# Optimization experiments

Hardware: AMD Instinct MI355X
Metric: run time of the kernel (lower is better)

## Reference

```python
import jax, jax.numpy as jnp
import numpy as np

D_MODEL = 1024
N_HEADS = 16
HEAD_DIM = D_MODEL // N_HEADS
BATCH = 2
SEQ = 2048


def setup_inputs() -> dict:
    key = jax.random.key(0)
    ks = jax.random.split(key, 9)
    s = 1.0 / np.sqrt(D_MODEL)
    x = jax.random.normal(ks[0], (BATCH, SEQ, D_MODEL), dtype=jnp.float32)
    # causal mask, broadcastable to (B, H, S, S); positions with 0 are masked out
    mask = jnp.tril(jnp.ones((SEQ, SEQ), dtype=bool))[None, None, :, :]
    Wq = jax.random.normal(ks[1], (D_MODEL, D_MODEL), dtype=jnp.float32) * s
    Wk = jax.random.normal(ks[2], (D_MODEL, D_MODEL), dtype=jnp.float32) * s
    Wv = jax.random.normal(ks[3], (D_MODEL, D_MODEL), dtype=jnp.float32) * s
    Wo = jax.random.normal(ks[4], (D_MODEL, D_MODEL), dtype=jnp.float32) * s
    bq = jnp.zeros((D_MODEL,), jnp.float32)
    bk = jnp.zeros((D_MODEL,), jnp.float32)
    bv = jnp.zeros((D_MODEL,), jnp.float32)
    bo = jnp.zeros((D_MODEL,), jnp.float32)
    return {"x": x, "mask": mask, "Wq": Wq, "bq": bq, "Wk": Wk, "bk": bk,
            "Wv": Wv, "bv": bv, "Wo": Wo, "bo": bo}


def reference(x, mask, Wq, bq, Wk, bk, Wv, bv, Wo, bo):
    B, S, _ = x.shape
    scale = HEAD_DIM ** -0.5
    # nn.Linear: y = x @ W.T + b ; W stored as (out, in)
    def proj(W, b):
        y = jnp.einsum('bsd,ed->bse', x, W) + b
        return y.reshape(B, S, N_HEADS, HEAD_DIM).transpose(0, 2, 1, 3)  # (B,H,S,Dh)
    q = proj(Wq, bq)
    k = proj(Wk, bk)
    v = proj(Wv, bv)
    scores = jnp.einsum('bhqd,bhkd->bhqk', q, k) * scale  # (B,H,S,S)
    scores = jnp.where(mask, scores, jnp.float32(-jnp.inf))
    weights = jax.nn.softmax(scores, axis=-1)
    attn = jnp.einsum('bhqk,bhkd->bhqd', weights, v)
    attn = attn.transpose(0, 2, 1, 3).reshape(B, S, D_MODEL)
    out = jnp.einsum('bsd,ed->bse', attn, Wo) + bo
    return out
```

## Files before the change

kernel.cpp:

```cpp
#include <hip/hip_runtime.h>
#include <hip/hip_bf16.h>

using bf16x8 = __attribute__((ext_vector_type(8))) short;
using f32x4  = __attribute__((ext_vector_type(4))) float;

#define SEQ      2048
#define DMODEL   1024
#define NHEADS   16
#define HDIM     64
#define MROWS    4096

__device__ __forceinline__ unsigned short f2bf(float f) {
  union { float f; unsigned u; } c; c.f = f;
  unsigned r = c.u + 0x7FFFu + ((c.u >> 16) & 1u);
  return (unsigned short)(r >> 16);
}

__device__ __forceinline__ unsigned cvtpk(float a, float b) {
  unsigned r;
  asm("v_cvt_pk_bf16_f32 %0, %1, %2" : "=v"(r) : "v"(a), "v"(b));
  return r;
}

__device__ __forceinline__ float fexp2(float x) {
  float r;
  asm("v_exp_f32 %0, %1" : "=v"(r) : "v"(x));
  return r;
}

__device__ __forceinline__ void gload16(const void* g, void* s) {
  __builtin_amdgcn_global_load_lds(
      (const __attribute__((address_space(1))) void*)g,
      (__attribute__((address_space(3))) void*)s, 16, 0, 0);
}

__global__ void cvt_all(const float* __restrict__ x,  const float* __restrict__ wq,
                        const float* __restrict__ wk, const float* __restrict__ wv,
                        const float* __restrict__ wo,
                        unsigned short* __restrict__ xb,  unsigned short* __restrict__ wqb,
                        unsigned short* __restrict__ wkb, unsigned short* __restrict__ wvb,
                        unsigned short* __restrict__ wob)
{
  int i = blockIdx.x * blockDim.x + threadIdx.x;
  const float* src; unsigned short* dst; int off;
  if (i < 1048576) { src = x; dst = xb; off = i; }
  else {
    int k = i - 1048576, seg = k >> 18; off = k & 262143;
    if      (seg == 0) { src = wq; dst = wqb; }
    else if (seg == 1) { src = wk; dst = wkb; }
    else if (seg == 2) { src = wv; dst = wvb; }
    else               { src = wo; dst = wob; }
  }
  const float4 v = ((const float4*)src)[off];
  ushort4 o;
  o.x = f2bf(v.x); o.y = f2bf(v.y); o.z = f2bf(v.z); o.w = f2bf(v.w);
  ((ushort4*)dst)[off] = o;
}

__global__ __launch_bounds__(256, 4)
void gemm_qkv(const unsigned short* __restrict__ Ab,
              const unsigned short* __restrict__ Wqb,
              const unsigned short* __restrict__ Wkb,
              const unsigned short* __restrict__ Wvb,
              const float* __restrict__ bq, const float* __restrict__ bk,
              const float* __restrict__ bv,
              unsigned short* __restrict__ Qo, unsigned short* __restrict__ Ko,
              unsigned short* __restrict__ Vto)
{
  __shared__ unsigned short Sbuf[2][128 * 64];
  unsigned short* As = Sbuf[0];
  unsigned short* Bs = Sbuf[1];
  const int t  = threadIdx.x;
  const int w  = t >> 6, l = t & 63;
  const int lr = l & 15, lg = l >> 4;
  const int bm = blockIdx.x / 24;
  const int bn = blockIdx.x % 24;
  const int which = bn >> 3;
  const unsigned short* Bsrc = which == 0 ? Wqb : (which == 1 ? Wkb : Wvb);
  const float* biasp = which == 0 ? bq : (which == 1 ? bk : bv);
  const int bnw = bn & 7;
  const int wm = w >> 1, wn = w & 1;

  const char* Agp = (const char*)Ab + (size_t)bm * 128 * 2048;
  const char* Bgp = (const char*)Bsrc + (size_t)bnw * 128 * 2048;

  f32x4 acc[4][4];
  #pragma unroll
  for (int a = 0; a < 4; ++a)
    #pragma unroll
    for (int b = 0; b < 4; ++b) acc[a][b] = (f32x4){0.f, 0.f, 0.f, 0.f};

  for (int kt = 0; kt < 16; ++kt) {
    const int kbyte = kt * 128;
    #pragma unroll
    for (int i = 0; i < 4; ++i) {
      int idx  = i * 256 + t;
      int row  = idx >> 3;
      int colb = (idx & 7) << 4;
      int scol = colb ^ ((row & 7) << 4);
      gload16(Agp + (size_t)row * 2048 + kbyte + scol, (char*)As + idx * 16);
      gload16(Bgp + (size_t)row * 2048 + kbyte + scol, (char*)Bs + idx * 16);
    }
    __syncthreads();
    #pragma unroll
    for (int kk = 0; kk < 2; ++kk) {
      bf16x8 af[4], bfr[4];
      #pragma unroll
      for (int x = 0; x < 4; ++x) {
        int ra = wm * 64 + x * 16 + lr;
        int rb = wn * 64 + x * 16 + lr;
        int cb = (kk * 64 + lg * 16) ^ ((lr & 7) << 4);
        af[x]  = *(const bf16x8*)((const char*)As + ra * 128 + cb);
        bfr[x] = *(const bf16x8*)((const char*)Bs + rb * 128 + cb);
      }
      #pragma unroll
      for (int xa = 0; xa < 4; ++xa)
        #pragma unroll
        for (int xb = 0; xb < 4; ++xb)
          acc[xa][xb] = __builtin_amdgcn_mfma_f32_16x16x32_bf16(af[xa], bfr[xb], acc[xa][xb], 0, 0, 0);
    }
    __syncthreads();
  }

  if (which == 2) {
    char* T = (char*)Sbuf;
    #pragma unroll
    for (int xb = 0; xb < 4; ++xb) {
      int col = wn * 64 + xb * 16 + lr;
      float biasv = biasp[bnw * 128 + col];
      #pragma unroll
      for (int xa = 0; xa < 4; ++xa) {
        int row0 = wm * 64 + xa * 16 + lg * 4;
        uint2 pk;
        pk.x = cvtpk(acc[xa][xb][0] + biasv, acc[xa][xb][1] + biasv);
        pk.y = cvtpk(acc[xa][xb][2] + biasv, acc[xa][xb][3] + biasv);
        *(uint2*)(T + col * 256 + (((row0 >> 3) ^ (col & 7)) << 4) + ((row0 & 7) << 1)) = pk;
      }
    }
    __syncthreads();
    const int bb = bm >> 4;
    const int s_base = (bm & 15) * 128;
    #pragma unroll
    for (int it = 0; it < 8; ++it) {
      int idx = it * 256 + t;
      int c   = idx >> 4;
      int sc  = idx & 15;
      uint4 v = *(const uint4*)(T + c * 256 + ((sc ^ (c & 7)) << 4));
      int colg = bnw * 128 + c;
      int h = colg >> 6, dh = colg & 63;
      int s0 = s_base + sc * 8;
      *(uint4*)&Vto[(((size_t)(bb * NHEADS + h)) * HDIM + dh) * SEQ + s0] = v;
    }
  } else {
    #pragma unroll
    for (int xb = 0; xb < 4; ++xb) {
      int colg = bnw * 128 + wn * 64 + xb * 16 + lr;
      int h  = colg >> 6, dh = colg & 63;
      float biasv = biasp[colg];
      #pragma unroll
      for (int xa = 0; xa < 4; ++xa) {
        int row0 = bm * 128 + wm * 64 + xa * 16 + lg * 4;
        #pragma unroll
        for (int i = 0; i < 4; ++i) {
          int m = row0 + i;
          int b = m >> 11, s = m & 2047;
          float v = acc[xa][xb][i] + biasv;
          if (which == 0)
            Qo[(((size_t)(b * NHEADS + h)) * SEQ + s) * HDIM + dh] = f2bf(v * 0.180336881f);
          else
            Ko[(((size_t)(b * NHEADS + h)) * SEQ + s) * HDIM + dh] = f2bf(v);
        }
      }
    }
  }
}

__device__ __forceinline__ void stage_kv64(const char* Kg, const char* Vg,
                                           char* Kl, char* Vl, int nb, int t)
{
  #pragma unroll
  for (int i = 0; i < 2; ++i) {
    int idx = i * 256 + t;
    int row = idx >> 3, colb = (idx & 7) << 4;
    int scol = colb ^ ((row & 7) << 4);
    gload16(Kg + (size_t)(nb + row) * 128 + scol, Kl + idx * 16);
    gload16(Vg + (size_t)row * 4096 + (size_t)nb * 2 + scol, Vl + idx * 16);
  }
}

__device__ __forceinline__ void attn_sub16(const char* Kl, const char* Vl, char* Pw,
                                           const bf16x8 (&qf)[2], const bf16x8 ones,
                                           f32x4 (&o)[4], f32x4 &accL,
                                           int q0w, int kbase, bool diag, int lr, int lg)
{
  bf16x8 kf[4][2];
  #pragma unroll
  for (int n = 0; n < 4; ++n)
    #pragma unroll
    for (int kk = 0; kk < 2; ++kk)
      kf[n][kk] = *(const bf16x8*)(Kl + (size_t)(n * 16 + lr) * 128 +
                                   ((kk * 64 + lg * 16) ^ ((lr & 7) << 4)));
  f32x4 st[4];
  __builtin_amdgcn_s_setprio(1);
  #pragma unroll
  for (int n = 0; n < 4; ++n) {
    f32x4 acc = (f32x4){0.f, 0.f, 0.f, 0.f};
    #pragma unroll
    for (int kk = 0; kk < 2; ++kk)
      acc = __builtin_amdgcn_mfma_f32_16x16x32_bf16(kf[n][kk], qf[kk], acc, 0, 0, 0);
    st[n] = acc;
  }
  __builtin_amdgcn_s_setprio(0);
  if (diag) {
    #pragma unroll
    for (int n = 0; n < 4; ++n) {
      #pragma unroll
      for (int i = 0; i < 4; ++i) {
        int key = kbase + n * 16 + lg * 4 + i;
        if (key > q0w + lr) st[n][i] = -3.0e38f;
      }
    }
  }
  #pragma unroll
  for (int n = 0; n < 4; ++n) {
    float p0 = fexp2(st[n][0]);
    float p1 = fexp2(st[n][1]);
    float p2 = fexp2(st[n][2]);
    float p3 = fexp2(st[n][3]);
    uint2 pw;
    pw.x = cvtpk(p0, p1);
    pw.y = cvtpk(p2, p3);
    *(uint2*)(Pw + lr * 128 + ((n * 32 + lg * 8) ^ ((lr & 7) << 4))) = pw;
  }
  __builtin_amdgcn_s_setprio(1);
  #pragma unroll
  for (int kk = 0; kk < 2; ++kk) {
    bf16x8 af = *(const bf16x8*)(Pw + lr * 128 + ((kk * 64 + lg * 16) ^ ((lr & 7) << 4)));
    accL = __builtin_amdgcn_mfma_f32_16x16x32_bf16(af, ones, accL, 0, 0, 0);
    #pragma unroll
    for (int n = 0; n < 4; ++n) {
      bf16x8 vf = *(const bf16x8*)(Vl + (size_t)(n * 16 + lr) * 128 +
                    ((kk * 64 + lg * 16) ^ ((lr & 7) << 4)));
      o[n] = __builtin_amdgcn_mfma_f32_16x16x32_bf16(af, vf, o[n], 0, 0, 0);
    }
  }
  __builtin_amdgcn_s_setprio(0);
}

__global__ __launch_bounds__(256, 2)
void attn_fwd(const unsigned short* __restrict__ Q,
              const unsigned short* __restrict__ K,
              const unsigned short* __restrict__ Vt,
              unsigned short* __restrict__ O)
{
  const int t = threadIdx.x;
  const int w = t >> 6, l = t & 63;
  const int lr = l & 15, lg = l >> 4;
  const int bh = blockIdx.x & 31;
  const int p  = blockIdx.x >> 5;
  const int qtA = p, qtB = 31 - p;
  const int b = bh >> 4, h = bh & 15;
  const int q0wA = qtA * 64 + w * 16;
  const int q0wB = qtB * 64 + w * 16;

  const unsigned short* Qp = Q + (size_t)bh * SEQ * HDIM;
  const char* Kg = (const char*)(K  + (size_t)bh * SEQ * HDIM);
  const char* Vg = (const char*)(Vt + (size_t)bh * HDIM * SEQ);

  __shared__ unsigned short Klds[2][64 * 64];
  __shared__ unsigned short Vlds[2][64 * 64];
  __shared__ unsigned short Plds[4][16][64];
  char* Pw = (char*)Plds[w];

  bf16x8 qfA[2], qfB[2];
  #pragma unroll
  for (int kk = 0; kk < 2; ++kk) {
    qfA[kk] = *(const bf16x8*)(Qp + (size_t)(q0wA + lr) * HDIM + kk * 32 + lg * 8);
    qfB[kk] = *(const bf16x8*)(Qp + (size_t)(q0wB + lr) * HDIM + kk * 32 + lg * 8);
  }

  bf16x8 ones;
  #pragma unroll
  for (int e = 0; e < 8; ++e) ones[e] = (short)0x3F80;

  f32x4 oA[4], oB[4];
  f32x4 accLA = (f32x4){0.f, 0.f, 0.f, 0.f};
  f32x4 accLB = (f32x4){0.f, 0.f, 0.f, 0.f};
  #pragma unroll
  for (int n = 0; n < 4; ++n) {
    oA[n] = (f32x4){0.f, 0.f, 0.f, 0.f};
    oB[n] = (f32x4){0.f, 0.f, 0.f, 0.f};
  }

  stage_kv64(Kg, Vg, (char*)Klds[0], (char*)Vlds[0], 0, t);
  {
    int kb1 = (1 <= qtA) ? 1 : 0;
    stage_kv64(Kg, Vg, (char*)Klds[1], (char*)Vlds[1], kb1 * 64, t);
  }

  int cur = 0;
  for (int j = 0; j < 33; ++j) {
    if (j < 32)
      asm volatile("s_waitcnt vmcnt(4)" ::: "memory");
    else
      asm volatile("s_waitcnt vmcnt(0)" ::: "memory");
    __builtin_amdgcn_s_barrier();
    asm volatile("" ::: "memory");
    if (j <= qtA) {
      attn_sub16((const char*)Klds[cur], (const char*)Vlds[cur], Pw, qfA, ones,
                 oA, accLA, q0wA, j * 64, j == qtA, lr, lg);
    } else {
      int kb = j - qtA - 1;
      attn_sub16((const char*)Klds[cur], (const char*)Vlds[cur], Pw, qfB, ones,
                 oB, accLB, q0wB, kb * 64, j == 32, lr, lg);
    }
    asm volatile("" ::: "memory");
    __builtin_amdgcn_s_barrier();
    asm volatile("" ::: "memory");
    if (j + 2 < 33) {
      int jn = j + 2;
      int kbn = (jn <= qtA) ? jn : jn - qtA - 1;
      stage_kv64(Kg, Vg, (char*)Klds[cur], (char*)Vlds[cur], kbn * 64, t);
    }
    cur ^= 1;
  }

  #pragma unroll
  for (int n = 0; n < 4; ++n) {
    int col = h * HDIM + n * 16 + lr;
    #pragma unroll
    for (int i = 0; i < 4; ++i) {
      int srowA = q0wA + lg * 4 + i;
      int srowB = q0wB + lg * 4 + i;
      O[((size_t)(b * SEQ + srowA)) * DMODEL + col] = f2bf(oA[n][i] / accLA[i]);
      O[((size_t)(b * SEQ + srowB)) * DMODEL + col] = f2bf(oB[n][i] / accLB[i]);
    }
  }
}

__global__ __launch_bounds__(256, 2)
void gemm_out(const unsigned short* __restrict__ Ab, const unsigned short* __restrict__ Bb,
              const float* __restrict__ bias, float* __restrict__ C)
{
  __shared__ unsigned short As[128 * 64];
  __shared__ unsigned short Bs[64 * 64];
  const int t  = threadIdx.x;
  const int w  = t >> 6, l = t & 63;
  const int lr = l & 15, lg = l >> 4;
  const int bm = blockIdx.x >> 4;
  const int bn = blockIdx.x & 15;
  const int wm = w >> 1, wn = w & 1;

  const char* Agp = (const char*)Ab + (size_t)bm * 128 * 2048;
  const char* Bgp = (const char*)Bb + (size_t)bn * 64 * 2048;

  f32x4 acc[4][2];
  #pragma unroll
  for (int a = 0; a < 4; ++a)
    #pragma unroll
    for (int b = 0; b < 2; ++b) acc[a][b] = (f32x4){0.f, 0.f, 0.f, 0.f};

  for (int kt = 0; kt < 16; ++kt) {
    const int kbyte = kt * 128;
    #pragma unroll
    for (int i = 0; i < 4; ++i) {
      int idx  = i * 256 + t;
      int row  = idx >> 3;
      int colb = (idx & 7) << 4;
      int scol = colb ^ ((row & 7) << 4);
      gload16(Agp + (size_t)row * 2048 + kbyte + scol, (char*)As + idx * 16);
    }
    #pragma unroll
    for (int i = 0; i < 2; ++i) {
      int idx  = i * 256 + t;
      int row  = idx >> 3;
      int colb = (idx & 7) << 4;
      int scol = colb ^ ((row & 7) << 4);
      gload16(Bgp + (size_t)row * 2048 + kbyte + scol, (char*)Bs + idx * 16);
    }
    __syncthreads();
    #pragma unroll
    for (int kk = 0; kk < 2; ++kk) {
      bf16x8 af[4], bfr[2];
      #pragma unroll
      for (int x = 0; x < 4; ++x) {
        int ra = wm * 64 + x * 16 + lr;
        int cb = (kk * 64 + lg * 16) ^ ((lr & 7) << 4);
        af[x]  = *(const bf16x8*)((const char*)As + ra * 128 + cb);
      }
      #pragma unroll
      for (int x = 0; x < 2; ++x) {
        int rb = wn * 32 + x * 16 + lr;
        int cb = (kk * 64 + lg * 16) ^ ((lr & 7) << 4);
        bfr[x] = *(const bf16x8*)((const char*)Bs + rb * 128 + cb);
      }
      #pragma unroll
      for (int xa = 0; xa < 4; ++xa)
        #pragma unroll
        for (int xb = 0; xb < 2; ++xb)
          acc[xa][xb] = __builtin_amdgcn_mfma_f32_16x16x32_bf16(af[xa], bfr[xb], acc[xa][xb], 0, 0, 0);
    }
    __syncthreads();
  }
  #pragma unroll
  for (int xb = 0; xb < 2; ++xb) {
    int col = bn * 64 + wn * 32 + xb * 16 + lr;
    float bvv = bias[col];
    #pragma unroll
    for (int xa = 0; xa < 4; ++xa) {
      int row0 = bm * 128 + wm * 64 + xa * 16 + lg * 4;
      #pragma unroll
      for (int i = 0; i < 4; ++i)
        C[(size_t)(row0 + i) * DMODEL + col] = acc[xa][xb][i] + bvv;
    }
  }
}

extern "C" void kernel_launch(void* const* d_in, const int* in_sizes, int n_in,
                              void* d_out, int out_size, void* d_ws, size_t ws_size,
                              hipStream_t stream)
{
  const float* x  = (const float*)d_in[0];
  const float* Wq = (const float*)d_in[2];
  const float* bq = (const float*)d_in[3];
  const float* Wk = (const float*)d_in[4];
  const float* bk = (const float*)d_in[5];
  const float* Wv = (const float*)d_in[6];
  const float* bv = (const float*)d_in[7];
  const float* Wo = (const float*)d_in[8];
  const float* bo = (const float*)d_in[9];

  char* ws = (char*)d_ws;
  const size_t MB = 1024 * 1024;
  unsigned short* xb   = (unsigned short*)(ws + 0);
  unsigned short* Wqb  = (unsigned short*)(ws + 8  * MB);
  unsigned short* Wkb  = (unsigned short*)(ws + 10 * MB);
  unsigned short* Wvb  = (unsigned short*)(ws + 12 * MB);
  unsigned short* Wob  = (unsigned short*)(ws + 14 * MB);
  unsigned short* Qb   = (unsigned short*)(ws + 16 * MB);
  unsigned short* Kb   = (unsigned short*)(ws + 24 * MB);
  unsigned short* Vtb  = (unsigned short*)(ws + 32 * MB);
  unsigned short* Attn = (unsigned short*)(ws + 40 * MB);

  cvt_all<<<8192, 256, 0, stream>>>(x, Wq, Wk, Wv, Wo, xb, Wqb, Wkb, Wvb, Wob);
  gemm_qkv<<<768, 256, 0, stream>>>(xb, Wqb, Wkb, Wvb, bq, bk, bv, Qb, Kb, Vtb);
  attn_fwd<<<512, 256, 0, stream>>>(Qb, Kb, Vtb, Attn);
  gemm_out<<<512, 256, 0, stream>>>(Attn, Wob, bo, (float*)d_out);
}
```

Before: 93.24 us.

## Split attention KV loop across two blocks and combine partial outputs

Each paired-tile attention block is split into two work items: one handles the short tile A plus the first part of tile B, the other handles the rest of tile B. Each writes unnormalized fp32 partial outputs and row sums, and a new combine kernel adds them and normalizes. This doubles the grid to 1024 blocks and raises the launch-bounds occupancy hint, aiming to fill more CUs and shorten the per-block serial loop. In exchange it adds an extra kernel launch plus fp32 partial-result traffic, and reuses workspace regions freed after the QKV GEMM (Wob is moved to avoid being overwritten).

Measured after the change: 93.11 us. No clear change (-0.1%).

```diff
diff --git a/kernel.cpp b/kernel.cpp
--- a/kernel.cpp
+++ b/kernel.cpp
@@ -247,17 +247,20 @@
   __builtin_amdgcn_s_setprio(0);
 }
 
-__global__ __launch_bounds__(256, 2)
+__global__ __launch_bounds__(256, 4)
 void attn_fwd(const unsigned short* __restrict__ Q,
               const unsigned short* __restrict__ K,
               const unsigned short* __restrict__ Vt,
-              unsigned short* __restrict__ O)
+              unsigned short* __restrict__ O,
+              float* __restrict__ O1, float* __restrict__ L1,
+              float* __restrict__ O2, float* __restrict__ L2)
 {
   const int t = threadIdx.x;
   const int w = t >> 6, l = t & 63;
   const int lr = l & 15, lg = l >> 4;
-  const int bh = blockIdx.x & 31;
-  const int p  = blockIdx.x >> 5;
+  const int bh   = blockIdx.x & 31;
+  const int p    = (blockIdx.x >> 5) & 15;
+  const int item = blockIdx.x >> 9;
   const int qtA = p, qtB = 31 - p;
   const int b = bh >> 4, h = bh & 15;
   const int q0wA = qtA * 64 + w * 16;
@@ -292,50 +295,98 @@
     oB[n] = (f32x4){0.f, 0.f, 0.f, 0.f};
   }
 
-  stage_kv64(Kg, Vg, (char*)Klds[0], (char*)Vlds[0], 0, t);
+  const int trips = (item == 0) ? 17 : 16;
+  const int ybase = 16 - p;
+
   {
-    int kb1 = (1 <= qtA) ? 1 : 0;
+    int kb0 = (item == 0) ? 0 : ybase;
+    int kb1 = (item == 0) ? ((1 <= p) ? 1 : 0) : (ybase + 1);
+    stage_kv64(Kg, Vg, (char*)Klds[0], (char*)Vlds[0], kb0 * 64, t);
     stage_kv64(Kg, Vg, (char*)Klds[1], (char*)Vlds[1], kb1 * 64, t);
   }
 
   int cur = 0;
-  for (int j = 0; j < 33; ++j) {
-    if (j < 32)
+  for (int j = 0; j < trips; ++j) {
+    if (j + 1 < trips)
       asm volatile("s_waitcnt vmcnt(4)" ::: "memory");
     else
       asm volatile("s_waitcnt vmcnt(0)" ::: "memory");
     __builtin_amdgcn_s_barrier();
     asm volatile("" ::: "memory");
-    if (j <= qtA) {
-      attn_sub16((const char*)Klds[cur], (const char*)Vlds[cur], Pw, qfA, ones,
-                 oA, accLA, q0wA, j * 64, j == qtA, lr, lg);
+    if (item == 0) {
+      if (j <= p) {
+        attn_sub16((const char*)Klds[cur], (const char*)Vlds[cur], Pw, qfA, ones,
+                   oA, accLA, q0wA, j * 64, j == p, lr, lg);
+      } else {
+        attn_sub16((const char*)Klds[cur], (const char*)Vlds[cur], Pw, qfB, ones,
+                   oB, accLB, q0wB, (j - p - 1) * 64, false, lr, lg);
+      }
     } else {
-      int kb = j - qtA - 1;
+      int kb = ybase + j;
       attn_sub16((const char*)Klds[cur], (const char*)Vlds[cur], Pw, qfB, ones,
-                 oB, accLB, q0wB, kb * 64, j == 32, lr, lg);
+                 oB, accLB, q0wB, kb * 64, kb == qtB, lr, lg);
     }
     asm volatile("" ::: "memory");
     __builtin_amdgcn_s_barrier();
     asm volatile("" ::: "memory");
-    if (j + 2 < 33) {
+    if (j + 2 < trips) {
       int jn = j + 2;
-      int kbn = (jn <= qtA) ? jn : jn - qtA - 1;
+      int kbn = (item == 0) ? ((jn <= p) ? jn : jn - p - 1) : (ybase + jn);
       stage_kv64(Kg, Vg, (char*)Klds[cur], (char*)Vlds[cur], kbn * 64, t);
     }
     cur ^= 1;
   }
 
-  #pragma unroll
-  for (int n = 0; n < 4; ++n) {
-    int col = h * HDIM + n * 16 + lr;
-    #pragma unroll
-    for (int i = 0; i < 4; ++i) {
-      int srowA = q0wA + lg * 4 + i;
-      int srowB = q0wB + lg * 4 + i;
-      O[((size_t)(b * SEQ + srowA)) * DMODEL + col] = f2bf(oA[n][i] / accLA[i]);
-      O[((size_t)(b * SEQ + srowB)) * DMODEL + col] = f2bf(oB[n][i] / accLB[i]);
-    }
-  }
+  if (item == 0) {
+    #pragma unroll
+    for (int n = 0; n < 4; ++n) {
+      int col = h * HDIM + n * 16 + lr;
+      #pragma unroll
+      for (int i = 0; i < 4; ++i) {
+        int srow = q0wA + lg * 4 + i;
+        O[((size_t)(b * SEQ + srow)) * DMODEL + col] = f2bf(oA[n][i] / accLA[i]);
+      }
+    }
+  }
+  {
+    float* Op = (item == 0) ? O1 : O2;
+    float* Lp = (item == 0) ? L1 : L2;
+    #pragma unroll
+    for (int n = 0; n < 4; ++n) {
+      int col = h * HDIM + n * 16 + lr;
+      #pragma unroll
+      for (int i = 0; i < 4; ++i) {
+        int srow = q0wB + lg * 4 + i;
+        int prow = b * 1024 + srow - 1024;
+        Op[(size_t)prow * DMODEL + col] = oB[n][i];
+      }
+    }
+    if (lr == 0) {
+      #pragma unroll
+      for (int i = 0; i < 4; ++i) {
+        int srow = q0wB + lg * 4 + i;
+        Lp[(b * 1024 + srow - 1024) * NHEADS + h] = accLB[i];
+      }
+    }
+  }
+}
+
+__global__ void attn_combine(const float* __restrict__ O1, const float* __restrict__ O2,
+                             const float* __restrict__ L1, const float* __restrict__ L2,
+                             unsigned short* __restrict__ Attn)
+{
+  int i = blockIdx.x * blockDim.x + threadIdx.x;
+  int col4 = i & 255;
+  int prow = i >> 8;
+  int b = prow >> 10, s = 1024 + (prow & 1023);
+  float4 a = ((const float4*)O1)[(size_t)prow * 256 + col4];
+  float4 c = ((const float4*)O2)[(size_t)prow * 256 + col4];
+  int h = col4 >> 4;
+  float inv = 1.0f / (L1[prow * NHEADS + h] + L2[prow * NHEADS + h]);
+  ushort4 u;
+  u.x = f2bf((a.x + c.x) * inv); u.y = f2bf((a.y + c.y) * inv);
+  u.z = f2bf((a.z + c.z) * inv); u.w = f2bf((a.w + c.w) * inv);
+  ((ushort4*)Attn)[(size_t)(b * SEQ + s) * 256 + col4] = u;
 }
 
 __global__ __launch_bounds__(256, 2)
@@ -436,14 +487,19 @@
   unsigned short* Wqb  = (unsigned short*)(ws + 8  * MB);
   unsigned short* Wkb  = (unsigned short*)(ws + 10 * MB);
   unsigned short* Wvb  = (unsigned short*)(ws + 12 * MB);
-  unsigned short* Wob  = (unsigned short*)(ws + 14 * MB);
   unsigned short* Qb   = (unsigned short*)(ws + 16 * MB);
   unsigned short* Kb   = (unsigned short*)(ws + 24 * MB);
   unsigned short* Vtb  = (unsigned short*)(ws + 32 * MB);
   unsigned short* Attn = (unsigned short*)(ws + 40 * MB);
+  unsigned short* Wob  = (unsigned short*)(ws + 48 * MB);
+  float*          L1   = (float*)(ws + 50 * MB);
+  float*          L2   = (float*)(ws + 50 * MB + 131072);
+  float*          O1   = (float*)(ws + 0);
+  float*          O2   = (float*)(ws + 8 * MB);
 
   cvt_all<<<8192, 256, 0, stream>>>(x, Wq, Wk, Wv, Wo, xb, Wqb, Wkb, Wvb, Wob);
   gemm_qkv<<<768, 256, 0, stream>>>(xb, Wqb, Wkb, Wvb, bq, bk, bv, Qb, Kb, Vtb);
-  attn_fwd<<<512, 256, 0, stream>>>(Qb, Kb, Vtb, Attn);
+  attn_fwd<<<1024, 256, 0, stream>>>(Qb, Kb, Vtb, Attn, O1, L1, O2, L2);
+  attn_combine<<<2048, 256, 0, stream>>>(O1, O2, L1, L2, Attn);
   gemm_out<<<512, 256, 0, stream>>>(Attn, Wob, bo, (float*)d_out);
 }
```
